# Performance work log

Measured on AMD Instinct MI355X. Metric: run time of the kernel, lower is better.

## Reference

```python
import jax, jax.numpy as jnp
import numpy as np

B, C, Hsp, Wsp = 16, 256, 64, 64
NUM_HEADS = 8
NORM_GROUPS = 4
EPS = 1e-5


def setup_inputs() -> dict:
    key = jax.random.key(0)
    ks = jax.random.split(key, 6)
    x = jax.random.normal(ks[0], (B, C, Hsp, Wsp), dtype=jnp.float32)
    gn_weight = jnp.ones((C,), dtype=jnp.float32)
    gn_bias = jnp.zeros((C,), dtype=jnp.float32)
    # Conv2d 1x1 kernels == dense matrices over channels
    qkv_weight = jax.random.normal(ks[1], (3 * C, C), dtype=jnp.float32) * (1.0 / np.sqrt(C))
    proj_weight = jax.random.normal(ks[2], (C, C), dtype=jnp.float32) * (1.0 / np.sqrt(C))
    proj_bias = jax.random.normal(ks[3], (C,), dtype=jnp.float32) * 0.01
    return {
        "x": x,
        "gn_weight": gn_weight,
        "gn_bias": gn_bias,
        "qkv_weight": qkv_weight,
        "proj_weight": proj_weight,
        "proj_bias": proj_bias,
    }


def reference(x, gn_weight, gn_bias, qkv_weight, proj_weight, proj_bias):
    b, c, h, w = x.shape
    hd = c // NUM_HEADS  # head dim
    n = h * w            # number of spatial tokens

    # GroupNorm over (c//G, h, w) per group, then per-channel affine
    xg = x.reshape(b, NORM_GROUPS, -1)
    mu = jnp.mean(xg, axis=-1, keepdims=True)
    var = jnp.mean(jnp.square(xg - mu), axis=-1, keepdims=True)
    xn = ((xg - mu) * jax.lax.rsqrt(var + EPS)).reshape(b, c, h, w)
    xn = xn * gn_weight[None, :, None, None] + gn_bias[None, :, None, None]

    # 1x1 conv (no bias) == channel matmul; output channel order matches torch view(b,3,H,d,h,w)
    qkv = jnp.einsum('bchw,oc->bohw', xn, qkv_weight)  # [b, 3c, h, w]
    qkv = qkv.reshape(b, 3, NUM_HEADS, hd, n)
    q, k, v = qkv[:, 0], qkv[:, 1], qkv[:, 2]          # each [b, H, d, n]

    # Linear (kernelized) attention: softmax over keys' token axis
    k = jax.nn.softmax(k, axis=-1)
    att = jnp.einsum('bhdn,bhen->bhde', k, v)          # [b, H, d, d]
    out = jnp.einsum('bhde,bhdn->bhen', att, q)        # [b, H, d, n]
    out = out.reshape(b, c, h, w)

    # Output 1x1 conv with bias
    return jnp.einsum('bchw,oc->bohw', out, proj_weight) + proj_bias[None, :, None, None]
```

## Files before the change

kernel.cpp:

```cpp
#include <hip/hip_runtime.h>
#include <hip/hip_bf16.h>


typedef __attribute__((ext_vector_type(4))) float f32x4;
typedef __attribute__((ext_vector_type(8))) short bf16x8;
typedef __attribute__((ext_vector_type(4))) short s16x4;
typedef __attribute__((ext_vector_type(8))) unsigned short u16x8;

__device__ inline float b2f(unsigned short u) {
  unsigned int x = ((unsigned int)u) << 16;
  float f; __builtin_memcpy(&f, &x, 4); return f;
}
__device__ inline unsigned short f2b(float f) {
  unsigned int x; __builtin_memcpy(&x, &f, 4);
  x += 0x7FFFu + ((x >> 16) & 1u);
  return (unsigned short)(x >> 16);
}

__global__ void __launch_bounds__(256) k_gn_partial(const float* __restrict__ x,
                                                    float* __restrict__ partials) {
  int blk = blockIdx.x;
  int grp = blk >> 4;
  int part = blk & 15;
  const float* base = x + (size_t)grp * 262144 + (size_t)part * 16384;
  int t = threadIdx.x;
  float s = 0.f, s2 = 0.f;
  for (int i = 0; i < 16; ++i) {
    f32x4 v = *(const f32x4*)(base + (size_t)(i * 256 + t) * 4);
    s  += v[0] + v[1] + v[2] + v[3];
    s2 += v[0]*v[0] + v[1]*v[1] + v[2]*v[2] + v[3]*v[3];
  }
  for (int o = 32; o > 0; o >>= 1) { s += __shfl_down(s, o); s2 += __shfl_down(s2, o); }
  __shared__ float ls[4], ls2[4];
  int w = t >> 6;
  if ((t & 63) == 0) { ls[w] = s; ls2[w] = s2; }
  __syncthreads();
  if (t == 0) {
    partials[blk * 2] = ls[0] + ls[1] + ls[2] + ls[3];
    partials[blk * 2 + 1] = ls2[0] + ls2[1] + ls2[2] + ls2[3];
  }
}

__global__ void __launch_bounds__(256) k_finalize(const float* __restrict__ partials,
                                                  float* __restrict__ stats,
                                                  const float* __restrict__ qkvw,
                                                  unsigned short* __restrict__ Wb,
                                                  unsigned short* __restrict__ WqT) {
  int bx = blockIdx.x, t = threadIdx.x;
  if (bx == 0) {
    if (t < 64) {
      float S = 0.f, S2 = 0.f;
      for (int i = 0; i < 16; ++i) { S += partials[(t * 16 + i) * 2]; S2 += partials[(t * 16 + i) * 2 + 1]; }
      float mu = S * (1.f / 262144.f);
      float var = S2 * (1.f / 262144.f) - mu * mu;
      stats[t * 2] = mu;
      stats[t * 2 + 1] = rsqrtf(var + 1e-5f);
    }
  } else if (bx <= 192) {
    int idx = (bx - 1) * 256 + t;
    int row = idx >> 6;
    float scl = (row >= 256 && row < 512) ? 1.4426950408889634f : 1.0f;
    f32x4 v = *(const f32x4*)(qkvw + (size_t)idx * 4);
    s16x4 o;
    for (int i = 0; i < 4; ++i) o[i] = (short)f2b(v[i] * scl);
    *(s16x4*)(Wb + (size_t)idx * 4) = o;
  } else {
    int bb = bx - 193;
    int c = bb * 16 + (t & 15);
    int d0 = (t >> 4) * 16;
    for (int i = 0; i < 16; ++i) {
      int d = d0 + i;
      WqT[(size_t)c * 256 + d] = f2b(qkvw[(size_t)d * 256 + c]);
    }
  }
}

__global__ void __launch_bounds__(256) k_norm_t(const float* __restrict__ x,
                                                const float* __restrict__ stats,
                                                const float* __restrict__ gamma,
                                                const float* __restrict__ beta,
                                                unsigned short* __restrict__ xnT) {
  int blk = blockIdx.x;
  int b = blk >> 8;
  int tile = blk & 255;
  int ct = tile >> 6;
  int nt = tile & 63;
  int c0 = ct * 64, n0 = nt * 64;
  __shared__ float T[64][65];
  int t = threadIdx.x;
  float mu = stats[(b * 4 + ct) * 2];
  float rs = stats[(b * 4 + ct) * 2 + 1];
  int cl = t >> 2, q4 = t & 3;
  float sc = gamma[c0 + cl] * rs;
  float off = beta[c0 + cl] - mu * sc;
  const float* xr = x + ((size_t)b * 256 + c0 + cl) * 4096 + n0;
  for (int p = 0; p < 4; ++p) {
    int col = p * 16 + q4 * 4;
    f32x4 v = *(const f32x4*)(xr + col);
    for (int i = 0; i < 4; ++i) T[cl][col + i] = v[i] * sc + off;
  }
  __syncthreads();
  int nl = t >> 2, cc = t & 3;
  u16x8 o0, o1;
  for (int i = 0; i < 8; ++i) o0[i] = f2b(T[cc * 16 + i][nl]);
  for (int i = 0; i < 8; ++i) o1[i] = f2b(T[cc * 16 + 8 + i][nl]);
  unsigned short* dst = xnT + ((size_t)b * 4096 + n0 + nl) * 256 + c0 + cc * 16;
  *(u16x8*)dst = o0;
  *(u16x8*)(dst + 8) = o1;
}

__global__ void __launch_bounds__(256, 2) k_attfused(const unsigned short* __restrict__ Wb,
                                                     const unsigned short* __restrict__ xnT,
                                                     float* __restrict__ attg,
                                                     float* __restrict__ rsums) {
  const int bx = blockIdx.x;
  const int b = bx >> 2, ns = bx & 3, h = blockIdx.y;
  const int hb = b * 8 + h;
  const int t = threadIdx.x;
  const int wave = t >> 6, lane = t & 63;
  const int g = lane >> 4, r = lane & 15;
  const int rh = wave >> 1;
  const int ch = wave & 1;
  __shared__ unsigned short XL[2][64][256];
  __shared__ unsigned short PL[32][72];
  __shared__ unsigned short VL[32][72];

  const unsigned short* Wrow = Wb + (size_t)(256 + rh * 256 + h * 32) * 256;
  bf16x8 af[2][8];
#pragma unroll
  for (int rt = 0; rt < 2; ++rt)
#pragma unroll
    for (int kt = 0; kt < 8; ++kt)
      af[rt][kt] = *(const bf16x8*)(Wrow + (size_t)(rt * 16 + r) * 256 + kt * 32 + 8 * g);

  const unsigned short* slice = xnT + ((size_t)b * 4096 + ns * 1024) * 256;
  const int swz = t >> 5;
  const unsigned short* gstage = slice + (size_t)swz * 256 + ((t & 31) ^ swz) * 8;
  char* lbase = (char*)&XL[0][0][0] + ((t >> 6) << 10);
#pragma unroll
  for (int i = 0; i < 8; ++i)
    __builtin_amdgcn_global_load_lds((const void*)(gstage + (size_t)(i * 8) * 256),
                                     (void*)(lbase + i * 4096), 16, 0, 0);

  f32x4 attacc = {0.f, 0.f, 0.f, 0.f};
  float rsm[2][4] = {{0.f,0.f,0.f,0.f},{0.f,0.f,0.f,0.f}};
  __syncthreads();

  for (int c = 0; c < 16; ++c) {
    const int cur = c & 1, nxt = cur ^ 1;
    if (c < 15) {
      const unsigned short* gs = gstage + (size_t)(c + 1) * 64 * 256;
      char* ld = lbase + (size_t)nxt * 32768;
#pragma unroll
      for (int i = 0; i < 8; ++i)
        __builtin_amdgcn_global_load_lds((const void*)(gs + (size_t)(i * 8) * 256),
                                         (void*)(ld + i * 4096), 16, 0, 0);
    }
    const char* xl0 = (const char*)&XL[cur][0][0];
    bf16x8 bfr[8][2];
#pragma unroll
    for (int kt = 0; kt < 8; ++kt)
#pragma unroll
      for (int ct = 0; ct < 2; ++ct) {
        const int row = ch * 32 + ct * 16 + r;
        const int slot = (kt * 4 + g) ^ (r & 7);
        bfr[kt][ct] = *(const bf16x8*)(xl0 + row * 512 + slot * 16);
      }
    f32x4 sacc[2][2] = {};
    __builtin_amdgcn_s_setprio(1);
#pragma unroll
    for (int kt = 0; kt < 8; ++kt) {
      sacc[0][0] = __builtin_amdgcn_mfma_f32_16x16x32_bf16(af[0][kt], bfr[kt][0], sacc[0][0], 0, 0, 0);
      sacc[0][1] = __builtin_amdgcn_mfma_f32_16x16x32_bf16(af[0][kt], bfr[kt][1], sacc[0][1], 0, 0, 0);
      sacc[1][0] = __builtin_amdgcn_mfma_f32_16x16x32_bf16(af[1][kt], bfr[kt][0], sacc[1][0], 0, 0, 0);
      sacc[1][1] = __builtin_amdgcn_mfma_f32_16x16x32_bf16(af[1][kt], bfr[kt][1], sacc[1][1], 0, 0, 0);
    }
    __builtin_amdgcn_s_setprio(0);
    unsigned short ov[2][2][4];
    if (rh == 0) {
#pragma unroll
      for (int rt = 0; rt < 2; ++rt)
#pragma unroll
        for (int ct = 0; ct < 2; ++ct)
#pragma unroll
          for (int reg = 0; reg < 4; ++reg) {
            float e = exp2f(sacc[rt][ct][reg]);
            rsm[rt][reg] += e;
            ov[rt][ct][reg] = f2b(e);
          }
    } else {
#pragma unroll
      for (int rt = 0; rt < 2; ++rt)
#pragma unroll
        for (int ct = 0; ct < 2; ++ct)
#pragma unroll
          for (int reg = 0; reg < 4; ++reg)
            ov[rt][ct][reg] = f2b(sacc[rt][ct][reg]);
    }
    __syncthreads();
    {
      unsigned short (*dstL)[72] = (rh == 0) ? PL : VL;
#pragma unroll
      for (int rt = 0; rt < 2; ++rt)
#pragma unroll
        for (int ct = 0; ct < 2; ++ct)
#pragma unroll
          for (int reg = 0; reg < 4; ++reg)
            dstL[rt * 16 + 4 * g + reg][ch * 32 + ct * 16 + r] = ov[rt][ct][reg];
    }
    __syncthreads();
#pragma unroll
    for (int ks = 0; ks < 2; ++ks) {
      bf16x8 pa = *(const bf16x8*)&PL[rh * 16 + r][ks * 32 + 8 * g];
      bf16x8 vb = *(const bf16x8*)&VL[ch * 16 + r][ks * 32 + 8 * g];
      attacc = __builtin_amdgcn_mfma_f32_16x16x32_bf16(pa, vb, attacc, 0, 0, 0);
    }
  }
  float* ab = attg + (size_t)hb * 1024;
#pragma unroll
  for (int reg = 0; reg < 4; ++reg)
    atomicAdd(&ab[(rh * 16 + 4 * g + reg) * 32 + ch * 16 + r], attacc[reg]);
  if (rh == 0) {
#pragma unroll
    for (int rt = 0; rt < 2; ++rt)
#pragma unroll
      for (int reg = 0; reg < 4; ++reg) {
        float v = rsm[rt][reg];
        v += __shfl_xor(v, 1); v += __shfl_xor(v, 2);
        v += __shfl_xor(v, 4); v += __shfl_xor(v, 8);
        if (r == 0) atomicAdd(&rsums[hb * 32 + rt * 16 + 4 * g + reg], v);
      }
  }
}

template<bool OUT_BF16, bool ADD_BIAS>
__global__ void __launch_bounds__(256)
k_gemm_bt(const unsigned short* __restrict__ A,
          const unsigned short* __restrict__ B,
          void* __restrict__ Cv,
          const float* __restrict__ bias,
          long sA, long sB, long sC, int ldc) {
  __shared__ unsigned short LA[128][32];
  __shared__ unsigned short LB[128][32];
  const int t = threadIdx.x;
  const unsigned short* Ab = A + (size_t)blockIdx.z * sA + (size_t)blockIdx.x * 128 * 256;
  const unsigned short* Bb = B + (size_t)blockIdx.z * sB + (size_t)blockIdx.y * 128 * 256;
  const int wave = t >> 6, lane = t & 63;
  const int wm = wave >> 1, wn = wave & 1;
  const int g = lane >> 4, r = lane & 15;
  const int rA = t >> 2, sslot = t & 3;
  const int ws0 = 8 * (sslot ^ (rA & 3));
  const int rslot = 8 * (g ^ (r & 3));
  const unsigned short* ag = Ab + (size_t)rA * 256 + 8 * sslot;
  const unsigned short* bg = Bb + (size_t)rA * 256 + 8 * sslot;
  u16x8 pa0 = *(const u16x8*)(ag);
  u16x8 pa1 = *(const u16x8*)(ag + 64 * 256);
  u16x8 pb0 = *(const u16x8*)(bg);
  u16x8 pb1 = *(const u16x8*)(bg + 64 * 256);
  f32x4 acc[4][4] = {};
  for (int kt = 0; kt < 8; ++kt) {
    if (kt) __syncthreads();
    *(u16x8*)&LA[rA][ws0] = pa0;  *(u16x8*)&LA[rA + 64][ws0] = pa1;
    *(u16x8*)&LB[rA][ws0] = pb0;  *(u16x8*)&LB[rA + 64][ws0] = pb1;
    __syncthreads();
    if (kt < 7) {
      int off = (kt + 1) * 32;
      pa0 = *(const u16x8*)(ag + off);  pa1 = *(const u16x8*)(ag + 64 * 256 + off);
      pb0 = *(const u16x8*)(bg + off);  pb1 = *(const u16x8*)(bg + 64 * 256 + off);
    }
    bf16x8 af[4], bfr[4];
    for (int i = 0; i < 4; ++i) {
      af[i]  = *(const bf16x8*)&LA[wm * 64 + i * 16 + r][rslot];
      bfr[i] = *(const bf16x8*)&LB[wn * 64 + i * 16 + r][rslot];
    }
    for (int mi = 0; mi < 4; ++mi)
      for (int ni = 0; ni < 4; ++ni)
        acc[mi][ni] = __builtin_amdgcn_mfma_f32_16x16x32_bf16(af[mi], bfr[ni], acc[mi][ni], 0, 0, 0);
  }
  const int m0 = blockIdx.x * 128 + wm * 64;
  const int n0 = blockIdx.y * 128 + wn * 64;
  if (OUT_BF16) {
    unsigned short* C = (unsigned short*)Cv + (size_t)blockIdx.z * sC;
    for (int mi = 0; mi < 4; ++mi)
      for (int ni = 0; ni < 4; ++ni) {
        int row = m0 + mi * 16 + 4 * g;
        int col = n0 + ni * 16 + r;
        for (int reg = 0; reg < 4; ++reg)
          C[(size_t)(row + reg) * ldc + col] = f2b(acc[mi][ni][reg]);
      }
  } else {
    float* C = (float*)Cv + (size_t)blockIdx.z * sC;
    for (int mi = 0; mi < 4; ++mi)
      for (int ni = 0; ni < 4; ++ni) {
        int row = m0 + mi * 16 + 4 * g;
        int col = n0 + ni * 16 + r;
        for (int reg = 0; reg < 4; ++reg) {
          float v = acc[mi][ni][reg];
          if (ADD_BIAS) v += bias[row + reg];
          C[(size_t)(row + reg) * ldc + col] = v;
        }
      }
  }
}

__global__ void __launch_bounds__(256) k_makeM(const float* __restrict__ attg,
                                               const float* __restrict__ rsums,
                                               const float* __restrict__ projw,
                                               unsigned short* __restrict__ Mb) {
  int blk = blockIdx.x;
  int b = blk >> 3, h = blk & 7;
  __shared__ float attL[32][33];
  __shared__ float invs[32];
  int t = threadIdx.x;
  if (t < 32) invs[t] = 1.f / rsums[blk * 32 + t];
  const float* asrc = attg + (size_t)blk * 1024;
  {
    f32x4 v = *(const f32x4*)(asrc + (size_t)t * 4);
    int idx = t * 4;
    for (int i = 0; i < 4; ++i) attL[(idx + i) >> 5][(idx + i) & 31] = v[i];
  }
  __syncthreads();
  float pw[32];
  const float* ps = projw + (size_t)t * 256 + h * 32;
  for (int i = 0; i < 8; ++i) {
    f32x4 v = *(const f32x4*)(ps + i * 4);
    pw[i * 4 + 0] = v[0]; pw[i * 4 + 1] = v[1]; pw[i * 4 + 2] = v[2]; pw[i * 4 + 3] = v[3];
  }
  unsigned short* dst = Mb + ((size_t)b * 256 + t) * 256 + h * 32;
  for (int dd = 0; dd < 32; ++dd) {
    float s = 0.f;
    for (int e = 0; e < 32; ++e) s += pw[e] * attL[dd][e];
    dst[dd] = f2b(s * invs[dd]);
  }
}

__global__ void __launch_bounds__(256) k_gemm_final(const unsigned short* __restrict__ M2,
                                                    const unsigned short* __restrict__ xnT,
                                                    float* __restrict__ out,
                                                    const float* __restrict__ bias) {
  const int nt = blockIdx.x, b = blockIdx.y;
  const unsigned short* Ab = M2 + (size_t)b * 65536;
  const unsigned short* Bb = xnT + ((size_t)b * 4096 + nt * 64) * 256;
  float* Cb = out + (size_t)b * 1048576 + (size_t)nt * 64;
  __shared__ unsigned short LB[2][64][32];
  const int t = threadIdx.x;
  const int wave = t >> 6, lane = t & 63, g = lane >> 4, r = lane & 15;
  const int srow = t >> 2, sslot = t & 3;
  const int ws0 = 8 * (sslot ^ (srow & 3));
  const int rslot = 8 * (g ^ (r & 3));
  const unsigned short* bg = Bb + (size_t)srow * 256 + 8 * sslot;
  const unsigned short* ar = Ab + (size_t)(wave * 64 + r) * 256 + 8 * g;
  u16x8 pb = *(const u16x8*)bg;
  f32x4 acc[4][4] = {};
  for (int kt = 0; kt < 8; ++kt) {
    const int cur = kt & 1;
    *(u16x8*)&LB[cur][srow][ws0] = pb;
    __syncthreads();
    if (kt < 7) pb = *(const u16x8*)(bg + (kt + 1) * 32);
    bf16x8 af[4], bfr[4];
#pragma unroll
    for (int mi = 0; mi < 4; ++mi)
      af[mi] = *(const bf16x8*)(ar + (size_t)(mi * 16) * 256 + kt * 32);
#pragma unroll
    for (int ni = 0; ni < 4; ++ni)
      bfr[ni] = *(const bf16x8*)&LB[cur][ni * 16 + r][rslot];
#pragma unroll
    for (int mi = 0; mi < 4; ++mi)
#pragma unroll
      for (int ni = 0; ni < 4; ++ni)
        acc[mi][ni] = __builtin_amdgcn_mfma_f32_16x16x32_bf16(af[mi], bfr[ni], acc[mi][ni], 0, 0, 0);
  }
#pragma unroll
  for (int mi = 0; mi < 4; ++mi) {
    const int row = wave * 64 + mi * 16 + 4 * g;
#pragma unroll
    for (int ni = 0; ni < 4; ++ni)
#pragma unroll
      for (int reg = 0; reg < 4; ++reg)
        Cb[(size_t)(row + reg) * 4096 + ni * 16 + r] = acc[mi][ni][reg] + bias[row + reg];
  }
}

extern "C" void kernel_launch(void* const* d_in, const int* in_sizes, int n_in,
                              void* d_out, int out_size, void* d_ws, size_t ws_size,
                              hipStream_t stream) {
  (void)in_sizes; (void)n_in; (void)out_size; (void)ws_size;
  const float* x     = (const float*)d_in[0];
  const float* gn_w  = (const float*)d_in[1];
  const float* gn_b  = (const float*)d_in[2];
  const float* qkvw  = (const float*)d_in[3];
  const float* projw = (const float*)d_in[4];
  const float* projb = (const float*)d_in[5];

  char* ws = (char*)d_ws;
  float*          partials = (float*)(ws);
  float*          stats    = (float*)(ws + 8192);
  unsigned short* Wb       = (unsigned short*)(ws + 16384);
  unsigned short* Mb       = (unsigned short*)(ws + 409600);
  float*          attg     = (float*)(ws + 2506752);
  float*          rsums    = (float*)(ws + 3031040);
  unsigned short* WqT      = (unsigned short*)(ws + 3047424);
  unsigned short* M2       = (unsigned short*)(ws + 3178496);
  unsigned short* xnT      = (unsigned short*)(ws + 8388608);

  k_gn_partial<<<1024, 256, 0, stream>>>(x, partials);
  k_finalize<<<209, 256, 0, stream>>>(partials, stats, qkvw, Wb, WqT);
  k_norm_t<<<4096, 256, 0, stream>>>(x, stats, gn_w, gn_b, xnT);
  (void)hipMemsetAsync(attg, 0, 540672, stream);
  k_attfused<<<dim3(64, 8), 256, 0, stream>>>(Wb, xnT, attg, rsums);
  k_makeM<<<128, 256, 0, stream>>>(attg, rsums, projw, Mb);
  k_gemm_bt<true, false><<<dim3(2, 2, 16), 256, 0, stream>>>(
      Mb, WqT, (void*)M2, nullptr, 65536L, 0L, 65536L, 256);
  k_gemm_final<<<dim3(64, 16), 256, 0, stream>>>(M2, xnT, (float*)d_out, projb);
}
```

Baseline: 210.2 us.

## Keep K/V projection outputs in registers and feed att MFMA directly

Each wave now computes K and V for its own 16 tokens, with tokens on the M dimension, so the MFMA output layout can be reused as the A/B operand of the attention MFMA without going through shared memory. Outputs from two consecutive chunks are packed into 8-element bf16 fragments, and att is accumulated per wave. The four wave partials are then reduced through LDS before one set of atomics. This removes the per-chunk LDS round trip and one barrier per iteration. In exchange it holds twice as many weight fragments in registers, which could lower occupancy.

```diff
diff --git a/kernel.cpp b/kernel.cpp
--- a/kernel.cpp
+++ b/kernel.cpp
@@ -119,19 +119,20 @@
   const int t = threadIdx.x;
   const int wave = t >> 6, lane = t & 63;
   const int g = lane >> 4, r = lane & 15;
-  const int rh = wave >> 1;
-  const int ch = wave & 1;
   __shared__ unsigned short XL[2][64][256];
-  __shared__ unsigned short PL[32][72];
-  __shared__ unsigned short VL[32][72];
-
-  const unsigned short* Wrow = Wb + (size_t)(256 + rh * 256 + h * 32) * 256;
-  bf16x8 af[2][8];
-#pragma unroll
-  for (int rt = 0; rt < 2; ++rt)
-#pragma unroll
-    for (int kt = 0; kt < 8; ++kt)
-      af[rt][kt] = *(const bf16x8*)(Wrow + (size_t)(rt * 16 + r) * 256 + kt * 32 + 8 * g);
+
+  bf16x8 wk[2][8], wv[2][8];
+  {
+    const unsigned short* Wk = Wb + (size_t)(256 + h * 32) * 256;
+    const unsigned short* Wv = Wb + (size_t)(512 + h * 32) * 256;
+#pragma unroll
+    for (int dt = 0; dt < 2; ++dt)
+#pragma unroll
+      for (int kt = 0; kt < 8; ++kt) {
+        wk[dt][kt] = *(const bf16x8*)(Wk + (size_t)(dt * 16 + r) * 256 + kt * 32 + 8 * g);
+        wv[dt][kt] = *(const bf16x8*)(Wv + (size_t)(dt * 16 + r) * 256 + kt * 32 + 8 * g);
+      }
+  }
 
   const unsigned short* slice = xnT + ((size_t)b * 4096 + ns * 1024) * 256;
   const int swz = t >> 5;
@@ -142,8 +143,10 @@
     __builtin_amdgcn_global_load_lds((const void*)(gstage + (size_t)(i * 8) * 256),
                                      (void*)(lbase + i * 4096), 16, 0, 0);
 
-  f32x4 attacc = {0.f, 0.f, 0.f, 0.f};
-  float rsm[2][4] = {{0.f,0.f,0.f,0.f},{0.f,0.f,0.f,0.f}};
+  f32x4 att[2][2] = {};
+  float rsum[2] = {0.f, 0.f};
+  s16x4 paE[2], vbE[2];
+  const char* xrow = (const char*)&XL[0][0][0] + (size_t)(wave * 16 + r) * 512;
   __syncthreads();
 
   for (int c = 0; c < 16; ++c) {
@@ -156,80 +159,82 @@
         __builtin_amdgcn_global_load_lds((const void*)(gs + (size_t)(i * 8) * 256),
                                          (void*)(ld + i * 4096), 16, 0, 0);
     }
-    const char* xl0 = (const char*)&XL[cur][0][0];
-    bf16x8 bfr[8][2];
+    const char* xr = xrow + (size_t)cur * 32768;
+    bf16x8 xf[8];
 #pragma unroll
     for (int kt = 0; kt < 8; ++kt)
-#pragma unroll
-      for (int ct = 0; ct < 2; ++ct) {
-        const int row = ch * 32 + ct * 16 + r;
-        const int slot = (kt * 4 + g) ^ (r & 7);
-        bfr[kt][ct] = *(const bf16x8*)(xl0 + row * 512 + slot * 16);
+      xf[kt] = *(const bf16x8*)(xr + (((kt * 4 + g) ^ (r & 7)) << 4));
+    f32x4 sacc[2] = {};
+    f32x4 vacc[2] = {};
+    __builtin_amdgcn_s_setprio(1);
+#pragma unroll
+    for (int kt = 0; kt < 8; ++kt) {
+      sacc[0] = __builtin_amdgcn_mfma_f32_16x16x32_bf16(xf[kt], wk[0][kt], sacc[0], 0, 0, 0);
+      sacc[1] = __builtin_amdgcn_mfma_f32_16x16x32_bf16(xf[kt], wk[1][kt], sacc[1], 0, 0, 0);
+      vacc[0] = __builtin_amdgcn_mfma_f32_16x16x32_bf16(xf[kt], wv[0][kt], vacc[0], 0, 0, 0);
+      vacc[1] = __builtin_amdgcn_mfma_f32_16x16x32_bf16(xf[kt], wv[1][kt], vacc[1], 0, 0, 0);
+    }
+    __builtin_amdgcn_s_setprio(0);
+    s16x4 pa[2], vb[2];
+#pragma unroll
+    for (int dt = 0; dt < 2; ++dt)
+#pragma unroll
+      for (int reg = 0; reg < 4; ++reg) {
+        float e = exp2f(sacc[dt][reg]);
+        rsum[dt] += e;
+        pa[dt][reg] = (short)f2b(e);
+        vb[dt][reg] = (short)f2b(vacc[dt][reg]);
       }
-    f32x4 sacc[2][2] = {};
-    __builtin_amdgcn_s_setprio(1);
-#pragma unroll
-    for (int kt = 0; kt < 8; ++kt) {
-      sacc[0][0] = __builtin_amdgcn_mfma_f32_16x16x32_bf16(af[0][kt], bfr[kt][0], sacc[0][0], 0, 0, 0);
-      sacc[0][1] = __builtin_amdgcn_mfma_f32_16x16x32_bf16(af[0][kt], bfr[kt][1], sacc[0][1], 0, 0, 0);
-      sacc[1][0] = __builtin_amdgcn_mfma_f32_16x16x32_bf16(af[1][kt], bfr[kt][0], sacc[1][0], 0, 0, 0);
-      sacc[1][1] = __builtin_amdgcn_mfma_f32_16x16x32_bf16(af[1][kt], bfr[kt][1], sacc[1][1], 0, 0, 0);
-    }
-    __builtin_amdgcn_s_setprio(0);
-    unsigned short ov[2][2][4];
-    if (rh == 0) {
-#pragma unroll
-      for (int rt = 0; rt < 2; ++rt)
-#pragma unroll
-        for (int ct = 0; ct < 2; ++ct)
-#pragma unroll
-          for (int reg = 0; reg < 4; ++reg) {
-            float e = exp2f(sacc[rt][ct][reg]);
-            rsm[rt][reg] += e;
-            ov[rt][ct][reg] = f2b(e);
-          }
+    if ((c & 1) == 0) {
+      paE[0] = pa[0]; paE[1] = pa[1];
+      vbE[0] = vb[0]; vbE[1] = vb[1];
     } else {
-#pragma unroll
-      for (int rt = 0; rt < 2; ++rt)
-#pragma unroll
-        for (int ct = 0; ct < 2; ++ct)
-#pragma unroll
-          for (int reg = 0; reg < 4; ++reg)
-            ov[rt][ct][reg] = f2b(sacc[rt][ct][reg]);
+      bf16x8 paf[2], vbf[2];
+#pragma unroll
+      for (int dt = 0; dt < 2; ++dt) {
+        paf[dt][0] = paE[dt][0]; paf[dt][1] = paE[dt][1];
+        paf[dt][2] = paE[dt][2]; paf[dt][3] = paE[dt][3];
+        paf[dt][4] = pa[dt][0];  paf[dt][5] = pa[dt][1];
+        paf[dt][6] = pa[dt][2];  paf[dt][7] = pa[dt][3];
+        vbf[dt][0] = vbE[dt][0]; vbf[dt][1] = vbE[dt][1];
+        vbf[dt][2] = vbE[dt][2]; vbf[dt][3] = vbE[dt][3];
+        vbf[dt][4] = vb[dt][0];  vbf[dt][5] = vb[dt][1];
+        vbf[dt][6] = vb[dt][2];  vbf[dt][7] = vb[dt][3];
+      }
+#pragma unroll
+      for (int dt = 0; dt < 2; ++dt)
+#pragma unroll
+        for (int et = 0; et < 2; ++et)
+          att[dt][et] = __builtin_amdgcn_mfma_f32_16x16x32_bf16(paf[dt], vbf[et], att[dt][et], 0, 0, 0);
     }
     __syncthreads();
-    {
-      unsigned short (*dstL)[72] = (rh == 0) ? PL : VL;
-#pragma unroll
-      for (int rt = 0; rt < 2; ++rt)
-#pragma unroll
-        for (int ct = 0; ct < 2; ++ct)
-#pragma unroll
-          for (int reg = 0; reg < 4; ++reg)
-            dstL[rt * 16 + 4 * g + reg][ch * 32 + ct * 16 + r] = ov[rt][ct][reg];
-    }
-    __syncthreads();
-#pragma unroll
-    for (int ks = 0; ks < 2; ++ks) {
-      bf16x8 pa = *(const bf16x8*)&PL[rh * 16 + r][ks * 32 + 8 * g];
-      bf16x8 vb = *(const bf16x8*)&VL[ch * 16 + r][ks * 32 + 8 * g];
-      attacc = __builtin_amdgcn_mfma_f32_16x16x32_bf16(pa, vb, attacc, 0, 0, 0);
-    }
-  }
+  }
+
+  float* XF = (float*)&XL[0][0][0];
+#pragma unroll
+  for (int dt = 0; dt < 2; ++dt)
+#pragma unroll
+    for (int et = 0; et < 2; ++et)
+#pragma unroll
+      for (int reg = 0; reg < 4; ++reg)
+        XF[wave * 1024 + (dt * 16 + 4 * g + reg) * 32 + et * 16 + r] = att[dt][et][reg];
+  __syncthreads();
   float* ab = attg + (size_t)hb * 1024;
-#pragma unroll
-  for (int reg = 0; reg < 4; ++reg)
-    atomicAdd(&ab[(rh * 16 + 4 * g + reg) * 32 + ch * 16 + r], attacc[reg]);
-  if (rh == 0) {
-#pragma unroll
-    for (int rt = 0; rt < 2; ++rt)
-#pragma unroll
-      for (int reg = 0; reg < 4; ++reg) {
-        float v = rsm[rt][reg];
-        v += __shfl_xor(v, 1); v += __shfl_xor(v, 2);
-        v += __shfl_xor(v, 4); v += __shfl_xor(v, 8);
-        if (r == 0) atomicAdd(&rsums[hb * 32 + rt * 16 + 4 * g + reg], v);
-      }
+  {
+    f32x4 s0 = *(f32x4*)&XF[t * 4];
+    f32x4 s1 = *(f32x4*)&XF[1024 + t * 4];
+    f32x4 s2 = *(f32x4*)&XF[2048 + t * 4];
+    f32x4 s3 = *(f32x4*)&XF[3072 + t * 4];
+#pragma unroll
+    for (int i = 0; i < 4; ++i)
+      atomicAdd(&ab[t * 4 + i], s0[i] + s1[i] + s2[i] + s3[i]);
+  }
+#pragma unroll
+  for (int dt = 0; dt < 2; ++dt) {
+    float v = rsum[dt];
+    v += __shfl_xor(v, 16);
+    v += __shfl_xor(v, 32);
+    if (g == 0) atomicAdd(&rsums[hb * 32 + dt * 16 + r], v);
   }
 }
 
```

Measured after the change: 207.7 us. About the same (-1.2%).
